# Performance work log

Measured on AMD Instinct MI355X. Metric: run time of the kernel, lower is better.

Reference implementation:

```python
import jax, jax.numpy as jnp
import numpy as np

H = 12  # num_attention_heads
DH = 64  # attention_head_size


def setup_inputs() -> dict:
    key = jax.random.key(0)
    ks = jax.random.split(key, 4)
    B, S, D = 2, 2048, 768
    sc = 1.0 / np.sqrt(D)
    return {
        "hidden_states": jax.random.normal(ks[0], (B, S, D), jnp.float32),
        "attention_mask": jnp.zeros((B, 1, 1, S), jnp.float32),
        "Wq": jax.random.normal(ks[1], (D, D), jnp.float32) * sc,
        "bq": jnp.zeros((D,), jnp.float32),
        "Wk": jax.random.normal(ks[2], (D, D), jnp.float32) * sc,
        "bk": jnp.zeros((D,), jnp.float32),
        "Wv": jax.random.normal(ks[3], (D, D), jnp.float32) * sc,
        "bv": jnp.zeros((D,), jnp.float32),
    }


def reference(hidden_states, attention_mask, Wq, bq, Wk, bk, Wv, bv):
    B, S, D = hidden_states.shape
    # Linear projections (nn.Linear: x @ W^T + b); weights stored here as [in, out]
    q = hidden_states @ Wq + bq
    k = hidden_states @ Wk + bk
    v = hidden_states @ Wv + bv
    # [B, S, D] -> [B, H, S, Dh]
    def split_heads(x):
        return x.reshape(B, S, H, DH).transpose(0, 2, 1, 3)
    q, k, v = split_heads(q), split_heads(k), split_heads(v)
    scores = jnp.einsum("bhqd,bhkd->bhqk", q, k) / jnp.sqrt(jnp.float32(DH))
    scores = scores + attention_mask  # broadcast [B,1,1,S] additive mask
    attention_softmax = jax.nn.softmax(scores, axis=-1)
    # dropout is identity in eval mode
    context = jnp.einsum("bhqk,bhkd->bhqd", attention_softmax, v)
    context = context.transpose(0, 2, 1, 3).reshape(B, S, H * DH)
    return (context, attention_softmax)
```

## Files before the change

kernel.cpp:

```cpp
#include <hip/hip_runtime.h>
#include <hip/hip_bf16.h>

#define S_LEN 2048
#define DM 768
#define NH 12
#define DH 64
#define BATCH 2
#define SC 0.1803368801111204f
#define LOG2E 1.4426950408889634f

typedef __attribute__((ext_vector_type(8))) short bf16x8;
typedef __attribute__((ext_vector_type(4))) float f32x4;
typedef __attribute__((ext_vector_type(16))) float f32x16;
typedef __attribute__((ext_vector_type(8))) unsigned short u16x8;

__device__ __forceinline__ unsigned short f2bf(float f) {
  union { float f; unsigned u; } v; v.f = f;
  unsigned r = (v.u + 0x7fffu + ((v.u >> 16) & 1u)) >> 16;
  return (unsigned short)r;
}
__device__ __forceinline__ unsigned cvt2(float a, float b) {
  __hip_bfloat162 h = __float22bfloat162_rn(float2{a, b});
  return *reinterpret_cast<unsigned*>(&h);
}

__global__ __launch_bounds__(256) void wtrans(
    const float* __restrict__ Wq, const float* __restrict__ Wk, const float* __restrict__ Wv,
    unsigned short* __restrict__ Wt)
{
  const int z = blockIdx.z;
  const float* W = (z == 0) ? Wq : (z == 1) ? Wk : Wv;
  const float sc = (z == 0) ? SC : 1.0f;
  __shared__ float Lt[64][65];
  const int t = threadIdx.x;
  const int row0 = blockIdx.y * 64, col0 = blockIdx.x * 64;
  const int r = t >> 2, c0 = (t & 3) * 16;
  const float4* src = (const float4*)(W + (size_t)(row0 + r) * DM + col0 + c0);
  #pragma unroll
  for (int j = 0; j < 4; ++j) {
    const float4 v = src[j];
    Lt[r][c0 + 4 * j] = v.x; Lt[r][c0 + 4 * j + 1] = v.y;
    Lt[r][c0 + 4 * j + 2] = v.z; Lt[r][c0 + 4 * j + 3] = v.w;
  }
  __syncthreads();
  const int nn = t >> 2, kk0 = (t & 3) * 16;
  unsigned wo[8];
  #pragma unroll
  for (int j = 0; j < 8; ++j)
    wo[j] = cvt2(Lt[kk0 + 2 * j][nn] * sc, Lt[kk0 + 2 * j + 1][nn] * sc);
  unsigned short* dst = Wt + ((size_t)(z * DM + col0 + nn)) * DM + row0 + kk0;
  *(uint4*)dst = *(uint4*)&wo[0];
  *(uint4*)(dst + 8) = *(uint4*)&wo[4];
}

#define BM 128
#define BN 128
#define BK 64
#define LDPAD 72

__global__ __launch_bounds__(256) void qkv_gemm(
    const float* __restrict__ X,
    const unsigned short* __restrict__ Wt,
    const float* __restrict__ bq, const float* __restrict__ bk, const float* __restrict__ bv,
    unsigned short* __restrict__ Qo, unsigned short* __restrict__ Kf,
    unsigned short* __restrict__ Vf)
{
  const int z = blockIdx.z;
  const float* bias = (z == 0) ? bq : (z == 1) ? bk : bv;
  const float bsc = (z == 0) ? SC : 1.0f;

  __shared__ __align__(16) unsigned short Al[BM][LDPAD];
  __shared__ __align__(16) unsigned short Bl[BN][LDPAD];

  const int t = threadIdx.x;
  const int wv = t >> 6, lane = t & 63;
  const int g = lane >> 4, c = lane & 15;
  const int wm = (wv >> 1) * 64, wn = (wv & 1) * 64;
  const int m0 = blockIdx.y * BM, n0 = blockIdx.x * BN;

  f32x4 acc[4][4];
  #pragma unroll
  for (int i = 0; i < 4; ++i)
    #pragma unroll
    for (int j = 0; j < 4; ++j) {
      float bb = bias[n0 + wn + j * 16 + c] * bsc;
      f32x4 a4 = {bb, bb, bb, bb};
      acc[i][j] = a4;
    }

  const int a_m = t >> 1, a_k = (t & 1) * 32;

  for (int kt = 0; kt < DM / BK; ++kt) {
    const int k0 = kt * BK;
    __syncthreads();
    #pragma unroll
    for (int half = 0; half < 2; ++half) {
      const float4* src = (const float4*)(X + (size_t)(m0 + a_m) * DM + k0 + a_k + 16 * half);
      const float4 x0 = src[0], x1 = src[1], x2 = src[2], x3 = src[3];
      uint4 v0 = {cvt2(x0.x, x0.y), cvt2(x0.z, x0.w), cvt2(x1.x, x1.y), cvt2(x1.z, x1.w)};
      uint4 v1 = {cvt2(x2.x, x2.y), cvt2(x2.z, x2.w), cvt2(x3.x, x3.y), cvt2(x3.z, x3.w)};
      *(uint4*)&Al[a_m][a_k + 16 * half] = v0;
      *(uint4*)&Al[a_m][a_k + 16 * half + 8] = v1;
    }
    {
      const unsigned short* srcB = Wt + ((size_t)(z * DM + n0 + a_m)) * DM + k0 + a_k;
      const u16x8 w0 = *(const u16x8*)srcB;
      const u16x8 w1 = *(const u16x8*)(srcB + 8);
      const u16x8 w2 = *(const u16x8*)(srcB + 16);
      const u16x8 w3 = *(const u16x8*)(srcB + 24);
      *(u16x8*)&Bl[a_m][a_k] = w0;
      *(u16x8*)&Bl[a_m][a_k + 8] = w1;
      *(u16x8*)&Bl[a_m][a_k + 16] = w2;
      *(u16x8*)&Bl[a_m][a_k + 24] = w3;
    }
    __syncthreads();
    #pragma unroll
    for (int kk = 0; kk < 2; ++kk) {
      bf16x8 af[4], bfr[4];
      #pragma unroll
      for (int i = 0; i < 4; ++i) af[i]  = *(const bf16x8*)&Al[wm + i * 16 + c][kk * 32 + 8 * g];
      #pragma unroll
      for (int j = 0; j < 4; ++j) bfr[j] = *(const bf16x8*)&Bl[wn + j * 16 + c][kk * 32 + 8 * g];
      #pragma unroll
      for (int i = 0; i < 4; ++i)
        #pragma unroll
        for (int j = 0; j < 4; ++j)
          acc[i][j] = __builtin_amdgcn_mfma_f32_16x16x32_bf16(af[i], bfr[j], acc[i][j], 0, 0, 0);
    }
  }

  if (z == 0) {
    #pragma unroll
    for (int i = 0; i < 4; ++i)
      #pragma unroll
      for (int j = 0; j < 4; ++j)
        #pragma unroll
        for (int r = 0; r < 4; ++r) {
          const int m = m0 + wm + i * 16 + 4 * g + r;
          const int n = n0 + wn + j * 16 + c;
          Qo[(size_t)m * DM + n] = f2bf(acc[i][j][r]);
        }
  } else if (z == 1) {
    #pragma unroll
    for (int i = 0; i < 4; ++i)
      #pragma unroll
      for (int j = 0; j < 4; ++j) {
        const int n = n0 + wn + j * 16 + c;
        const int h = n >> 6, d = n & 63, ch = d >> 3, e = d & 7;
        #pragma unroll
        for (int r = 0; r < 4; ++r) {
          const int m = m0 + wm + i * 16 + 4 * g + r;
          const int b = m >> 11, s = m & 2047;
          const int st = s >> 5, r32 = s & 31;
          const size_t w = (((size_t)(b * NH + h) * 64 + st) * 8 + ch) * 32 + r32;
          Kf[w * 8 + e] = f2bf(acc[i][j][r]);
        }
      }
  } else {
    #pragma unroll
    for (int i = 0; i < 4; ++i)
      #pragma unroll
      for (int j = 0; j < 4; ++j) {
        const int n = n0 + wn + j * 16 + c;
        const int h = n >> 6, d = n & 63;
        const int mb = m0 + wm + i * 16 + 4 * g;
        const int b = mb >> 11, s = mb & 2047;
        const int kk = s >> 3, j0 = s & 7;
        unsigned short* dst = &Vf[(((size_t)(b * NH + h) * 256 + kk) * 64 + d) * 8 + j0];
        uint2 pk = {cvt2(acc[i][j][0], acc[i][j][1]), cvt2(acc[i][j][2], acc[i][j][3])};
        *(uint2*)dst = pk;
      }
  }
}

__global__ __launch_bounds__(256, 3) void attn_fused(
    const unsigned short* __restrict__ Qb,
    const bf16x8* __restrict__ Kf,
    const bf16x8* __restrict__ Vf,
    const float* __restrict__ mask,
    float* __restrict__ ctx,
    float* __restrict__ Pout)
{
  const int bid = blockIdx.x;
  const int wg = (bid & 7) * 192 + (bid >> 3);
  const int qt = wg & 63;
  const int bh = wg >> 6;
  const int b = bh / NH, h = bh % NH;

  const int t = threadIdx.x, wv = t >> 6, lane = t & 63;
  const int q = lane & 31, hi = lane >> 5;
  const int q0 = qt * 32;

  __shared__ __align__(16) float Pf[4][32][36];
  __shared__ __align__(16) float Osum[32][68];
  __shared__ float mlb[4][32];

  bf16x8 bqf[4];
  {
    const unsigned short* qp = Qb + (size_t)(b * S_LEN + q0 + q) * DM + h * DH + 8 * hi;
    #pragma unroll
    for (int m = 0; m < 4; ++m) bqf[m] = *(const bf16x8*)(qp + 16 * m);
  }

  const bf16x8* kfb = Kf + ((size_t)bh * 64 + wv * 16) * 256;
  const bf16x8* vfb = Vf + ((size_t)bh * 256 + wv * 64) * 64;
  const float* mrow = mask + (size_t)b * S_LEN + wv * 512;

  float ll = 0.f;

  bf16x8 kc[4];
  #pragma unroll
  for (int m = 0; m < 4; ++m) kc[m] = kfb[(2 * m + hi) * 32 + q];

  for (int st = 0; st < 16; ++st) {
    bf16x8 kn[4];
    const int stn = (st + 1) & 15;
    #pragma unroll
    for (int m = 0; m < 4; ++m) kn[m] = kfb[stn * 256 + (2 * m + hi) * 32 + q];

    f32x16 s;
    #pragma unroll
    for (int rg = 0; rg < 4; ++rg) {
      const f32x4 mk = *(const f32x4*)&mrow[st * 32 + 8 * rg + 4 * hi];
      #pragma unroll
      for (int ri = 0; ri < 4; ++ri) s[4 * rg + ri] = mk[ri] * LOG2E;
    }
    #pragma unroll
    for (int m = 0; m < 4; ++m)
      s = __builtin_amdgcn_mfma_f32_32x32x16_bf16(kc[m], bqf[m], s, 0, 0, 0);

    float e[16];
    #pragma unroll
    for (int r = 0; r < 16; ++r) e[r] = __builtin_amdgcn_exp2f(s[r]);
    const float t0 = (e[0] + e[1]) + (e[2] + e[3]);
    const float t1 = (e[4] + e[5]) + (e[6] + e[7]);
    const float t2 = (e[8] + e[9]) + (e[10] + e[11]);
    const float t3 = (e[12] + e[13]) + (e[14] + e[15]);
    ll += (t0 + t1) + (t2 + t3);
    #pragma unroll
    for (int m = 0; m < 4; ++m) kc[m] = kn[m];
  }
  ll += __shfl_xor(ll, 32);
  if (hi == 0) mlb[wv][q] = ll;
  __syncthreads();

  const float lsum = (mlb[0][q] + mlb[1][q]) + (mlb[2][q] + mlb[3][q]);
  const float mfin = __builtin_amdgcn_logf(lsum);

  f32x16 o0, o1;
  #pragma unroll
  for (int r = 0; r < 16; ++r) { o0[r] = 0.f; o1[r] = 0.f; }

  float* pbase = Pout + (size_t)bh * S_LEN * S_LEN + (size_t)q0 * S_LEN + wv * 512;
  const int sr = lane >> 3, scl = lane & 7;

  for (int st = 0; st < 16; ++st) {
    bf16x8 kn[4];
    const int stn = (st + 1) & 15;
    #pragma unroll
    for (int m = 0; m < 4; ++m) kn[m] = kfb[stn * 256 + (2 * m + hi) * 32 + q];

    const bf16x8 vb00 = vfb[(st * 4 + hi) * 64 + q];
    const bf16x8 vb01 = vfb[(st * 4 + hi) * 64 + 32 + q];
    const bf16x8 vb10 = vfb[(st * 4 + 2 + hi) * 64 + q];
    const bf16x8 vb11 = vfb[(st * 4 + 2 + hi) * 64 + 32 + q];

    f32x16 s;
    #pragma unroll
    for (int rg = 0; rg < 4; ++rg) {
      const f32x4 mk = *(const f32x4*)&mrow[st * 32 + 8 * rg + 4 * hi];
      #pragma unroll
      for (int ri = 0; ri < 4; ++ri) s[4 * rg + ri] = mk[ri] * LOG2E;
    }
    #pragma unroll
    for (int m = 0; m < 4; ++m)
      s = __builtin_amdgcn_mfma_f32_32x32x16_bf16(kc[m], bqf[m], s, 0, 0, 0);

    #pragma unroll
    for (int r = 0; r < 16; ++r) s[r] = __builtin_amdgcn_exp2f(s[r] - mfin);

    #pragma unroll
    for (int rg = 0; rg < 4; ++rg) {
      f32x4 pv = {s[4 * rg], s[4 * rg + 1], s[4 * rg + 2], s[4 * rg + 3]};
      *(f32x4*)&Pf[wv][q][8 * rg + 4 * hi] = pv;
    }

    unsigned c0 = cvt2(s[0], s[1]),   c1 = cvt2(s[2], s[3]);
    unsigned c2 = cvt2(s[4], s[5]),   c3 = cvt2(s[6], s[7]);
    unsigned c4 = cvt2(s[8], s[9]),   c5 = cvt2(s[10], s[11]);
    unsigned c6 = cvt2(s[12], s[13]), c7 = cvt2(s[14], s[15]);
    auto r02 = __builtin_amdgcn_permlane32_swap(c0, c2, false, false);
    auto r13 = __builtin_amdgcn_permlane32_swap(c1, c3, false, false);
    auto r46 = __builtin_amdgcn_permlane32_swap(c4, c6, false, false);
    auto r57 = __builtin_amdgcn_permlane32_swap(c5, c7, false, false);
    uint4 u0 = {r02[0], r13[0], r02[1], r13[1]};
    uint4 u1 = {r46[0], r57[0], r46[1], r57[1]};
    const bf16x8 pa0 = *reinterpret_cast<bf16x8*>(&u0);
    const bf16x8 pa1 = *reinterpret_cast<bf16x8*>(&u1);

    o0 = __builtin_amdgcn_mfma_f32_32x32x16_bf16(pa0, vb00, o0, 0, 0, 0);
    o0 = __builtin_amdgcn_mfma_f32_32x32x16_bf16(pa1, vb10, o0, 0, 0, 0);
    o1 = __builtin_amdgcn_mfma_f32_32x32x16_bf16(pa0, vb01, o1, 0, 0, 0);
    o1 = __builtin_amdgcn_mfma_f32_32x32x16_bf16(pa1, vb11, o1, 0, 0, 0);

    asm volatile("s_waitcnt lgkmcnt(0)" ::: "memory");
    float* pst = pbase + st * 32;
    #pragma unroll
    for (int i = 0; i < 4; ++i) {
      const f32x4 row = *(const f32x4*)&Pf[wv][sr + 8 * i][scl * 4];
      *(f32x4*)(pst + (size_t)(sr + 8 * i) * S_LEN + scl * 4) = row;
    }
    #pragma unroll
    for (int m = 0; m < 4; ++m) kc[m] = kn[m];
  }

  #pragma unroll
  for (int w = 0; w < 4; ++w) {
    if (wv == w) {
      #pragma unroll
      for (int rg = 0; rg < 4; ++rg)
        #pragma unroll
        for (int ri = 0; ri < 4; ++ri) {
          const int qr = ri + 8 * rg + 4 * hi;
          if (w == 0) {
            Osum[qr][q]      = o0[4 * rg + ri];
            Osum[qr][32 + q] = o1[4 * rg + ri];
          } else {
            Osum[qr][q]      += o0[4 * rg + ri];
            Osum[qr][32 + q] += o1[4 * rg + ri];
          }
        }
    }
    __syncthreads();
  }

  const int row = t >> 3, d0 = (t & 7) * 8;
  const f32x4 r0 = *(const f32x4*)&Osum[row][d0];
  const f32x4 r1 = *(const f32x4*)&Osum[row][d0 + 4];
  float* crow = ctx + (size_t)(b * S_LEN + q0 + row) * DM + h * DH + d0;
  *(f32x4*)crow = r0;
  *(f32x4*)(crow + 4) = r1;
}

extern "C" void kernel_launch(void* const* d_in, const int* in_sizes, int n_in,
                              void* d_out, int out_size, void* d_ws, size_t ws_size,
                              hipStream_t stream) {
  const float* hs   = (const float*)d_in[0];
  const float* mask = (const float*)d_in[1];
  const float* Wq = (const float*)d_in[2];
  const float* bq = (const float*)d_in[3];
  const float* Wk = (const float*)d_in[4];
  const float* bk = (const float*)d_in[5];
  const float* Wv = (const float*)d_in[6];
  const float* bv = (const float*)d_in[7];

  const size_t MT = (size_t)BATCH * S_LEN * DM;
  unsigned short* Qb = (unsigned short*)d_ws;
  unsigned short* Kf = Qb + MT;
  unsigned short* Vf = Kf + MT;
  unsigned short* Wt = Vf + MT;

  float* ctx  = (float*)d_out;
  float* Pout = ctx + MT;

  wtrans<<<dim3(12, 12, 3), 256, 0, stream>>>(Wq, Wk, Wv, Wt);
  qkv_gemm<<<dim3(DM / BN, (BATCH * S_LEN) / BM, 3), 256, 0, stream>>>(
      hs, Wt, bq, bk, bv, Qb, Kf, Vf);
  attn_fused<<<dim3((S_LEN / 32) * NH * BATCH), 256, 0, stream>>>(
      Qb, (const bf16x8*)Kf, (const bf16x8*)Vf, mask, ctx, Pout);
}
```

Before: 182.9 us.

## Shrink QKV GEMM tile and drop K prefetch to raise occupancy

Halves the QKV GEMM M-tile from 128 to 64 rows, with each of the four waves now covering 64x32 instead of 64x64, and asks for 4 blocks per CU. This doubles the grid and cuts accumulator registers per thread. In the attention kernel's second pass, the next-tile K register prefetch is removed so K is loaded for the current tile, and launch bounds go from 3 to 4 blocks per CU. The aim is higher occupancy to hide latency, at the cost of less operand reuse in the GEMM and exposed K load latency in attention.

```diff
diff --git a/kernel.cpp b/kernel.cpp
--- a/kernel.cpp
+++ b/kernel.cpp
@@ -53,12 +53,12 @@
   *(uint4*)(dst + 8) = *(uint4*)&wo[4];
 }
 
-#define BM 128
+#define BM 64
 #define BN 128
 #define BK 64
 #define LDPAD 72
 
-__global__ __launch_bounds__(256) void qkv_gemm(
+__global__ __launch_bounds__(256, 4) void qkv_gemm(
     const float* __restrict__ X,
     const unsigned short* __restrict__ Wt,
     const float* __restrict__ bq, const float* __restrict__ bk, const float* __restrict__ bv,
@@ -75,56 +75,56 @@
   const int t = threadIdx.x;
   const int wv = t >> 6, lane = t & 63;
   const int g = lane >> 4, c = lane & 15;
-  const int wm = (wv >> 1) * 64, wn = (wv & 1) * 64;
+  const int wn = wv * 32;
   const int m0 = blockIdx.y * BM, n0 = blockIdx.x * BN;
 
-  f32x4 acc[4][4];
+  f32x4 acc[4][2];
   #pragma unroll
   for (int i = 0; i < 4; ++i)
     #pragma unroll
-    for (int j = 0; j < 4; ++j) {
+    for (int j = 0; j < 2; ++j) {
       float bb = bias[n0 + wn + j * 16 + c] * bsc;
       f32x4 a4 = {bb, bb, bb, bb};
       acc[i][j] = a4;
     }
 
-  const int a_m = t >> 1, a_k = (t & 1) * 32;
+  const int a_m = t >> 2, a_k = (t & 3) * 16;
+  const int b_n = t >> 1, b_k = (t & 1) * 32;
 
   for (int kt = 0; kt < DM / BK; ++kt) {
     const int k0 = kt * BK;
     __syncthreads();
-    #pragma unroll
-    for (int half = 0; half < 2; ++half) {
-      const float4* src = (const float4*)(X + (size_t)(m0 + a_m) * DM + k0 + a_k + 16 * half);
+    {
+      const float4* src = (const float4*)(X + (size_t)(m0 + a_m) * DM + k0 + a_k);
       const float4 x0 = src[0], x1 = src[1], x2 = src[2], x3 = src[3];
       uint4 v0 = {cvt2(x0.x, x0.y), cvt2(x0.z, x0.w), cvt2(x1.x, x1.y), cvt2(x1.z, x1.w)};
       uint4 v1 = {cvt2(x2.x, x2.y), cvt2(x2.z, x2.w), cvt2(x3.x, x3.y), cvt2(x3.z, x3.w)};
-      *(uint4*)&Al[a_m][a_k + 16 * half] = v0;
-      *(uint4*)&Al[a_m][a_k + 16 * half + 8] = v1;
+      *(uint4*)&Al[a_m][a_k] = v0;
+      *(uint4*)&Al[a_m][a_k + 8] = v1;
     }
     {
-      const unsigned short* srcB = Wt + ((size_t)(z * DM + n0 + a_m)) * DM + k0 + a_k;
+      const unsigned short* srcB = Wt + ((size_t)(z * DM + n0 + b_n)) * DM + k0 + b_k;
       const u16x8 w0 = *(const u16x8*)srcB;
       const u16x8 w1 = *(const u16x8*)(srcB + 8);
       const u16x8 w2 = *(const u16x8*)(srcB + 16);
       const u16x8 w3 = *(const u16x8*)(srcB + 24);
-      *(u16x8*)&Bl[a_m][a_k] = w0;
-      *(u16x8*)&Bl[a_m][a_k + 8] = w1;
-      *(u16x8*)&Bl[a_m][a_k + 16] = w2;
-      *(u16x8*)&Bl[a_m][a_k + 24] = w3;
+      *(u16x8*)&Bl[b_n][b_k] = w0;
+      *(u16x8*)&Bl[b_n][b_k + 8] = w1;
+      *(u16x8*)&Bl[b_n][b_k + 16] = w2;
+      *(u16x8*)&Bl[b_n][b_k + 24] = w3;
     }
     __syncthreads();
     #pragma unroll
     for (int kk = 0; kk < 2; ++kk) {
-      bf16x8 af[4], bfr[4];
-      #pragma unroll
-      for (int i = 0; i < 4; ++i) af[i]  = *(const bf16x8*)&Al[wm + i * 16 + c][kk * 32 + 8 * g];
-      #pragma unroll
-      for (int j = 0; j < 4; ++j) bfr[j] = *(const bf16x8*)&Bl[wn + j * 16 + c][kk * 32 + 8 * g];
+      bf16x8 af[4], bfr[2];
+      #pragma unroll
+      for (int i = 0; i < 4; ++i) af[i]  = *(const bf16x8*)&Al[i * 16 + c][kk * 32 + 8 * g];
+      #pragma unroll
+      for (int j = 0; j < 2; ++j) bfr[j] = *(const bf16x8*)&Bl[wn + j * 16 + c][kk * 32 + 8 * g];
       #pragma unroll
       for (int i = 0; i < 4; ++i)
         #pragma unroll
-        for (int j = 0; j < 4; ++j)
+        for (int j = 0; j < 2; ++j)
           acc[i][j] = __builtin_amdgcn_mfma_f32_16x16x32_bf16(af[i], bfr[j], acc[i][j], 0, 0, 0);
     }
   }
@@ -133,10 +133,10 @@
     #pragma unroll
     for (int i = 0; i < 4; ++i)
       #pragma unroll
-      for (int j = 0; j < 4; ++j)
+      for (int j = 0; j < 2; ++j)
         #pragma unroll
         for (int r = 0; r < 4; ++r) {
-          const int m = m0 + wm + i * 16 + 4 * g + r;
+          const int m = m0 + i * 16 + 4 * g + r;
           const int n = n0 + wn + j * 16 + c;
           Qo[(size_t)m * DM + n] = f2bf(acc[i][j][r]);
         }
@@ -144,12 +144,12 @@
     #pragma unroll
     for (int i = 0; i < 4; ++i)
       #pragma unroll
-      for (int j = 0; j < 4; ++j) {
+      for (int j = 0; j < 2; ++j) {
         const int n = n0 + wn + j * 16 + c;
         const int h = n >> 6, d = n & 63, ch = d >> 3, e = d & 7;
         #pragma unroll
         for (int r = 0; r < 4; ++r) {
-          const int m = m0 + wm + i * 16 + 4 * g + r;
+          const int m = m0 + i * 16 + 4 * g + r;
           const int b = m >> 11, s = m & 2047;
           const int st = s >> 5, r32 = s & 31;
           const size_t w = (((size_t)(b * NH + h) * 64 + st) * 8 + ch) * 32 + r32;
@@ -160,10 +160,10 @@
     #pragma unroll
     for (int i = 0; i < 4; ++i)
       #pragma unroll
-      for (int j = 0; j < 4; ++j) {
+      for (int j = 0; j < 2; ++j) {
         const int n = n0 + wn + j * 16 + c;
         const int h = n >> 6, d = n & 63;
-        const int mb = m0 + wm + i * 16 + 4 * g;
+        const int mb = m0 + i * 16 + 4 * g;
         const int b = mb >> 11, s = mb & 2047;
         const int kk = s >> 3, j0 = s & 7;
         unsigned short* dst = &Vf[(((size_t)(b * NH + h) * 256 + kk) * 64 + d) * 8 + j0];
@@ -173,7 +173,7 @@
   }
 }
 
-__global__ __launch_bounds__(256, 3) void attn_fused(
+__global__ __launch_bounds__(256, 4) void attn_fused(
     const unsigned short* __restrict__ Qb,
     const bf16x8* __restrict__ Kf,
     const bf16x8* __restrict__ Vf,
@@ -255,11 +255,9 @@
   const int sr = lane >> 3, scl = lane & 7;
 
   for (int st = 0; st < 16; ++st) {
-    bf16x8 kn[4];
-    const int stn = (st + 1) & 15;
-    #pragma unroll
-    for (int m = 0; m < 4; ++m) kn[m] = kfb[stn * 256 + (2 * m + hi) * 32 + q];
-
+    bf16x8 kcur[4];
+    #pragma unroll
+    for (int m = 0; m < 4; ++m) kcur[m] = kfb[st * 256 + (2 * m + hi) * 32 + q];
     const bf16x8 vb00 = vfb[(st * 4 + hi) * 64 + q];
     const bf16x8 vb01 = vfb[(st * 4 + hi) * 64 + 32 + q];
     const bf16x8 vb10 = vfb[(st * 4 + 2 + hi) * 64 + q];
@@ -274,7 +272,7 @@
     }
     #pragma unroll
     for (int m = 0; m < 4; ++m)
-      s = __builtin_amdgcn_mfma_f32_32x32x16_bf16(kc[m], bqf[m], s, 0, 0, 0);
+      s = __builtin_amdgcn_mfma_f32_32x32x16_bf16(kcur[m], bqf[m], s, 0, 0, 0);
 
     #pragma unroll
     for (int r = 0; r < 16; ++r) s[r] = __builtin_amdgcn_exp2f(s[r] - mfin);
@@ -310,8 +308,6 @@
       const f32x4 row = *(const f32x4*)&Pf[wv][sr + 8 * i][scl * 4];
       *(f32x4*)(pst + (size_t)(sr + 8 * i) * S_LEN + scl * 4) = row;
     }
-    #pragma unroll
-    for (int m = 0; m < 4; ++m) kc[m] = kn[m];
   }
 
   #pragma unroll
```

Result: slower. 195.6 us (+6.9%).
